# Kernel optimization log

Measured on AMD Instinct MI355X. Metric: run time of the kernel, lower is better.

Reference implementation:

```python
import jax, jax.numpy as jnp
import numpy as np

H = 10  # hidden_dim

def _lstm_layer(x_tbd, w_ih, w_hh, b_ih, b_hh):
    # x_tbd: [T, B, D]; w_ih: [4H, D]; w_hh: [4H, H]; biases [4H]
    B = x_tbd.shape[1]
    h0 = jnp.zeros((B, H), x_tbd.dtype)
    c0 = jnp.zeros((B, H), x_tbd.dtype)
    # precompute input projections for all timesteps: [T, B, 4H]
    xg = jnp.einsum('tbd,gd->tbg', x_tbd, w_ih) + b_ih + b_hh

    def step(carry, xg_t):
        h, c = carry
        gates = xg_t + h @ w_hh.T  # [B, 4H]
        i, f, g, o = jnp.split(gates, 4, axis=-1)  # torch gate order i,f,g,o
        i = jax.nn.sigmoid(i); f = jax.nn.sigmoid(f)
        g = jnp.tanh(g); o = jax.nn.sigmoid(o)
        c = f * c + i * g
        h = o * jnp.tanh(c)
        return (h, c), h

    (hT, cT), hs = jax.lax.scan(step, (h0, c0), xg)
    return hs, hT  # hs: [T, B, H]

def setup_inputs() -> dict:
    key = jax.random.key(0)
    ks = jax.random.split(key, 11)
    B, T, D = 32768, 28, 28
    s0 = 1.0 / np.sqrt(H)
    u = lambda k, shape: jax.random.uniform(k, shape, jnp.float32, -s0, s0)
    return {
        'x': jax.random.normal(ks[0], (B, T, D), jnp.float32),
        'w_ih0': u(ks[1], (4 * H, D)),
        'w_hh0': u(ks[2], (4 * H, H)),
        'b_ih0': u(ks[3], (4 * H,)),
        'b_hh0': u(ks[4], (4 * H,)),
        'w_ih1': u(ks[5], (4 * H, H)),
        'w_hh1': u(ks[6], (4 * H, H)),
        'b_ih1': u(ks[7], (4 * H,)),
        'b_hh1': u(ks[8], (4 * H,)),
        'w_cls': u(ks[9], (10, H)),
        'b_cls': u(ks[10], (10,)),
    }

def reference(x, w_ih0, w_hh0, b_ih0, b_hh0, w_ih1, w_hh1, b_ih1, b_hh1, w_cls, b_cls):
    x_tbd = jnp.swapaxes(x, 0, 1)  # [T, B, D]
    hs0, _ = _lstm_layer(x_tbd, w_ih0, w_hh0, b_ih0, b_hh0)
    _, hT1 = _lstm_layer(hs0, w_ih1, w_hh1, b_ih1, b_hh1)  # hT1 = h_n[-1]
    return hT1 @ w_cls.T + b_cls  # [B, 10]
```

## Files before the change

### kernel.cpp

```cpp
#include <hip/hip_runtime.h>


#define HDIM 10
#define DDIM 28
#define TSTEPS 28

typedef __attribute__((ext_vector_type(8))) short short8;
typedef __attribute__((ext_vector_type(4))) float f32x4;

__device__ __forceinline__ unsigned short bf16_rne(float f) {
    unsigned u = __builtin_bit_cast(unsigned, f);
    u += 0x7FFFu + ((u >> 16) & 1u);
    return (unsigned short)(u >> 16);
}
__device__ __forceinline__ float bf16_f(unsigned short h) {
    unsigned u = ((unsigned)h) << 16;
    return __builtin_bit_cast(float, u);
}
__device__ __forceinline__ unsigned pk_hl(float v) {
    unsigned a, p;
    const float z = 0.0f;
    asm("v_cvt_pk_bf16_f32 %0, %1, %2" : "=v"(a) : "v"(v), "v"(z));
    const float hif = __builtin_bit_cast(float, a << 16);
    const float d = v - hif;
    asm("v_cvt_pk_bf16_f32 %0, %1, %2" : "=v"(p) : "v"(v), "v"(d));
    return p;
}
__device__ __forceinline__ float sig_f(float v) {
    return __builtin_amdgcn_rcpf(1.0f + __expf(-v));
}
__device__ __forceinline__ float act_eval(float v, float a) {
    return a * __builtin_amdgcn_rcpf(1.0f + __expf(-a * v)) + (1.0f - a);
}
__device__ __forceinline__ float tanh_f(float v) {
    return 2.0f * __builtin_amdgcn_rcpf(1.0f + __expf(-2.0f * v)) - 1.0f;
}

#define FENCE() __asm volatile("" ::: "memory")
#define WR32(arrp, sidx, val) (*(unsigned*)&(arrp)[(sidx)] = (val))

__global__ __launch_bounds__(64) void lstm2_mfma_kernel(
    const float* __restrict__ x,
    const float* __restrict__ w_ih0, const float* __restrict__ w_hh0,
    const float* __restrict__ b_ih0, const float* __restrict__ b_hh0,
    const float* __restrict__ w_ih1, const float* __restrict__ w_hh1,
    const float* __restrict__ b_ih1, const float* __restrict__ b_hh1,
    const float* __restrict__ w_cls, const float* __restrict__ b_cls,
    float* __restrict__ out)
{
    __shared__ unsigned short uA0[16 * 136];
    __shared__ unsigned short uA1[16 * 72];
    __shared__ float gb[2][48 * 20];
    __shared__ float hfin[16 * 12];

    const int l  = threadIdx.x;
    const int lm = l & 15;
    const int q  = l >> 4;
    const int sbase = blockIdx.x * 16;

    for (int i = l; i < 16 * 22; i += 64) uA0[(i / 22) * 136 + 114 + (i % 22)] = 0;
    for (int i = l; i < 16 * 12; i += 64) uA1[(i / 12) * 72 + 60 + (i % 12)] = 0;

    short8 B0[3][4], B1[3][2];
    #pragma unroll
    for (int T = 0; T < 3; ++T) {
        const int n = lm + 16 * T;
        #pragma unroll
        for (int c = 0; c < 4; ++c) {
            #pragma unroll
            for (int j = 0; j < 8; ++j) {
                const int kk = 32 * c + 8 * q + j;
                unsigned short bits = 0;
                if (n < 40 && kk < 114) {
                    if (kk < 76) {
                        const int j2 = kk >> 1;
                        const float w = (j2 < 28) ? w_ih0[n * 28 + j2]
                                                  : w_hh0[n * 10 + (j2 - 28)];
                        bits = bf16_rne(w);
                    } else {
                        const int d = kk - 76;
                        const float w = (d < 28) ? w_ih0[n * 28 + d]
                                                 : w_hh0[n * 10 + (d - 28)];
                        const unsigned short hi = bf16_rne(w);
                        bits = bf16_rne(w - bf16_f(hi));
                    }
                }
                B0[T][c][j] = (short)bits;
            }
        }
        #pragma unroll
        for (int c = 0; c < 2; ++c) {
            #pragma unroll
            for (int j = 0; j < 8; ++j) {
                const int kk = 32 * c + 8 * q + j;
                unsigned short bits = 0;
                if (n < 40 && kk < 60) {
                    if (kk < 40) {
                        const int j2 = kk >> 1;
                        const float w = (j2 < 10) ? w_ih1[n * 10 + j2]
                                                  : w_hh1[n * 10 + (j2 - 10)];
                        bits = bf16_rne(w);
                    } else {
                        const int d = kk - 40;
                        const float w = (d < 10) ? w_ih1[n * 10 + d]
                                                 : w_hh1[n * 10 + (d - 10)];
                        const unsigned short hi = bf16_rne(w);
                        bits = bf16_rne(w - bf16_f(hi));
                    }
                }
                B1[T][c][j] = (short)bits;
            }
        }
    }

    float bias0[3], bias1[3];
    #pragma unroll
    for (int T = 0; T < 3; ++T) {
        const int n = lm + 16 * T;
        bias0[T] = (n < 40) ? (b_ih0[n] + b_hh0[n]) : 0.0f;
        bias1[T] = (n < 40) ? (b_ih1[n] + b_hh1[n]) : 0.0f;
    }
    const float a1v = (lm >= 4 && lm < 14) ? 2.0f : 1.0f;

    int xoff[7], lofsA[7], lofsB[7]; float xn[7];
    #pragma unroll
    for (int i = 0; i < 7; ++i) {
        const int f = l + 64 * i;
        const int sm = f / 28, d = f - 28 * sm;
        lofsA[i] = sm * 136 + 2 * d;
        lofsB[i] = sm * 136 + 76 + d;
        xoff[i] = (sbase + sm) * (TSTEPS * DDIM) + d;
        xn[i] = x[xoff[i]];
    }
    #pragma unroll
    for (int i = 0; i < 7; ++i) {
        const unsigned p = pk_hl(xn[i]);
        WR32(uA0, lofsA[i], p);
        uA0[lofsB[i]] = (unsigned short)p;
    }
    if (lm < 10) {
        #pragma unroll
        for (int r = 0; r < 4; ++r) {
            const int m = 4 * q + r;
            unsigned short* r0 = &uA0[m * 136];
            WR32(r0, 56 + 2 * lm, 0u); r0[104 + lm] = 0;
            unsigned short* r1 = &uA1[m * 72];
            WR32(r1, 2 * lm, 0u);      r1[40 + lm] = 0;
            WR32(r1, 20 + 2 * lm, 0u); r1[50 + lm] = 0;
        }
    }
    FENCE();

    float c0s[4] = {0, 0, 0, 0}, c1s[4] = {0, 0, 0, 0};
    float h1v[4] = {0, 0, 0, 0};
    float h0v[4];
    short8 A0f[4], A1f[2];
    float* const gb0 = gb[0];
    float* const gb1 = gb[1];

    #pragma unroll
    for (int c = 0; c < 4; ++c)
        A0f[c] = *(const short8*)&uA0[lm * 136 + 32 * c + 8 * q];
    FENCE();
    #pragma unroll
    for (int i = 0; i < 7; ++i) { xoff[i] += DDIM; xn[i] = x[xoff[i]]; }
    {
        f32x4 C[3];
        #pragma unroll
        for (int T = 0; T < 3; ++T) {
            f32x4 acc = {bias0[T], bias0[T], bias0[T], bias0[T]};
            #pragma unroll
            for (int c = 0; c < 4; ++c)
                acc = __builtin_amdgcn_mfma_f32_16x16x32_bf16(A0f[c], B0[T][c], acc, 0, 0, 0);
            C[T] = acc;
        }
        f32x4 g0, g1t, g2;
        #pragma unroll
        for (int r = 0; r < 4; ++r) {
            g0[r]  = sig_f(C[0][r]);
            g1t[r] = act_eval(C[1][r], a1v);
            g2[r]  = sig_f(C[2][r]);
        }
        *(f32x4*)&gb0[(lm     ) * 20 + 4 * q] = g0;
        *(f32x4*)&gb0[(lm + 16) * 20 + 4 * q] = g1t;
        *(f32x4*)&gb0[(lm + 32) * 20 + 4 * q] = g2;
    }
    FENCE();
    {
        const f32x4 iv = *(const f32x4*)&gb0[(lm     ) * 20 + 4 * q];
        const f32x4 fv = *(const f32x4*)&gb0[(lm + 10) * 20 + 4 * q];
        const f32x4 gg = *(const f32x4*)&gb0[(lm + 20) * 20 + 4 * q];
        const f32x4 ov = *(const f32x4*)&gb0[(lm + 30) * 20 + 4 * q];
        #pragma unroll
        for (int r = 0; r < 4; ++r) {
            const float c = fv[r] * c0s[r] + iv[r] * gg[r];
            c0s[r] = c;
            h0v[r] = ov[r] * tanh_f(c);
        }
        if (lm < 10) {
            #pragma unroll
            for (int r = 0; r < 4; ++r) {
                const int m = 4 * q + r;
                const unsigned p0 = pk_hl(h0v[r]);
                unsigned short* r0 = &uA0[m * 136];
                WR32(r0, 56 + 2 * lm, p0); r0[104 + lm] = (unsigned short)p0;
                unsigned short* r1 = &uA1[m * 72];
                WR32(r1, 2 * lm, p0);      r1[40 + lm] = (unsigned short)p0;
            }
        }
        #pragma unroll
        for (int i = 0; i < 7; ++i) {
            const unsigned p = pk_hl(xn[i]);
            WR32(uA0, lofsA[i], p);
            uA0[lofsB[i]] = (unsigned short)p;
        }
    }
    FENCE();

    #pragma unroll 1
    for (int t = 0; t < TSTEPS - 1; ++t) {
        #pragma unroll
        for (int c = 0; c < 2; ++c)
            A1f[c] = *(const short8*)&uA1[lm * 72 + 32 * c + 8 * q];
        #pragma unroll
        for (int c = 0; c < 4; ++c)
            A0f[c] = *(const short8*)&uA0[lm * 136 + 32 * c + 8 * q];
        FENCE();

        if (t < TSTEPS - 2) {
            #pragma unroll
            for (int i = 0; i < 7; ++i) { xoff[i] += DDIM; xn[i] = x[xoff[i]]; }
        }

        f32x4 C[3], D[3];
        #pragma unroll
        for (int T = 0; T < 3; ++T) {
            f32x4 accD = {bias1[T], bias1[T], bias1[T], bias1[T]};
            #pragma unroll
            for (int c = 0; c < 2; ++c)
                accD = __builtin_amdgcn_mfma_f32_16x16x32_bf16(A1f[c], B1[T][c], accD, 0, 0, 0);
            D[T] = accD;
            f32x4 accC = {bias0[T], bias0[T], bias0[T], bias0[T]};
            #pragma unroll
            for (int c = 0; c < 4; ++c)
                accC = __builtin_amdgcn_mfma_f32_16x16x32_bf16(A0f[c], B0[T][c], accC, 0, 0, 0);
            C[T] = accC;
        }

        {
            f32x4 d0, d1, d2, e0, e1, e2;
            #pragma unroll
            for (int r = 0; r < 4; ++r) {
                d0[r] = sig_f(D[0][r]);
                d1[r] = act_eval(D[1][r], a1v);
                d2[r] = sig_f(D[2][r]);
                e0[r] = sig_f(C[0][r]);
                e1[r] = act_eval(C[1][r], a1v);
                e2[r] = sig_f(C[2][r]);
            }
            *(f32x4*)&gb1[(lm     ) * 20 + 4 * q] = d0;
            *(f32x4*)&gb1[(lm + 16) * 20 + 4 * q] = d1;
            *(f32x4*)&gb1[(lm + 32) * 20 + 4 * q] = d2;
            *(f32x4*)&gb0[(lm     ) * 20 + 4 * q] = e0;
            *(f32x4*)&gb0[(lm + 16) * 20 + 4 * q] = e1;
            *(f32x4*)&gb0[(lm + 32) * 20 + 4 * q] = e2;
        }
        FENCE();

        {
            const f32x4 iv1 = *(const f32x4*)&gb1[(lm     ) * 20 + 4 * q];
            const f32x4 fv1 = *(const f32x4*)&gb1[(lm + 10) * 20 + 4 * q];
            const f32x4 gg1 = *(const f32x4*)&gb1[(lm + 20) * 20 + 4 * q];
            const f32x4 ov1 = *(const f32x4*)&gb1[(lm + 30) * 20 + 4 * q];
            const f32x4 iv0 = *(const f32x4*)&gb0[(lm     ) * 20 + 4 * q];
            const f32x4 fv0 = *(const f32x4*)&gb0[(lm + 10) * 20 + 4 * q];
            const f32x4 gg0 = *(const f32x4*)&gb0[(lm + 20) * 20 + 4 * q];
            const f32x4 ov0 = *(const f32x4*)&gb0[(lm + 30) * 20 + 4 * q];
            #pragma unroll
            for (int r = 0; r < 4; ++r) {
                const float c1 = fv1[r] * c1s[r] + iv1[r] * gg1[r];
                c1s[r] = c1;
                h1v[r] = ov1[r] * tanh_f(c1);
                const float c0 = fv0[r] * c0s[r] + iv0[r] * gg0[r];
                c0s[r] = c0;
                h0v[r] = ov0[r] * tanh_f(c0);
            }
            if (lm < 10) {
                #pragma unroll
                for (int r = 0; r < 4; ++r) {
                    const int m = 4 * q + r;
                    const unsigned p1 = pk_hl(h1v[r]);
                    unsigned short* r1 = &uA1[m * 72];
                    WR32(r1, 20 + 2 * lm, p1); r1[50 + lm] = (unsigned short)p1;
                    const unsigned p0 = pk_hl(h0v[r]);
                    WR32(r1, 2 * lm, p0);      r1[40 + lm] = (unsigned short)p0;
                    unsigned short* r0 = &uA0[m * 136];
                    WR32(r0, 56 + 2 * lm, p0); r0[104 + lm] = (unsigned short)p0;
                }
            }
            if (t < TSTEPS - 2) {
                #pragma unroll
                for (int i = 0; i < 7; ++i) {
                    const unsigned p = pk_hl(xn[i]);
                    WR32(uA0, lofsA[i], p);
                    uA0[lofsB[i]] = (unsigned short)p;
                }
            }
        }
        FENCE();
    }

    {
        #pragma unroll
        for (int c = 0; c < 2; ++c)
            A1f[c] = *(const short8*)&uA1[lm * 72 + 32 * c + 8 * q];
        FENCE();
        f32x4 D[3];
        #pragma unroll
        for (int T = 0; T < 3; ++T) {
            f32x4 acc = {bias1[T], bias1[T], bias1[T], bias1[T]};
            #pragma unroll
            for (int c = 0; c < 2; ++c)
                acc = __builtin_amdgcn_mfma_f32_16x16x32_bf16(A1f[c], B1[T][c], acc, 0, 0, 0);
            D[T] = acc;
        }
        f32x4 d0, d1, d2;
        #pragma unroll
        for (int r = 0; r < 4; ++r) {
            d0[r] = sig_f(D[0][r]);
            d1[r] = act_eval(D[1][r], a1v);
            d2[r] = sig_f(D[2][r]);
        }
        *(f32x4*)&gb1[(lm     ) * 20 + 4 * q] = d0;
        *(f32x4*)&gb1[(lm + 16) * 20 + 4 * q] = d1;
        *(f32x4*)&gb1[(lm + 32) * 20 + 4 * q] = d2;
        FENCE();
        const f32x4 iv = *(const f32x4*)&gb1[(lm     ) * 20 + 4 * q];
        const f32x4 fv = *(const f32x4*)&gb1[(lm + 10) * 20 + 4 * q];
        const f32x4 gg = *(const f32x4*)&gb1[(lm + 20) * 20 + 4 * q];
        const f32x4 ov = *(const f32x4*)&gb1[(lm + 30) * 20 + 4 * q];
        #pragma unroll
        for (int r = 0; r < 4; ++r) {
            const float c = fv[r] * c1s[r] + iv[r] * gg[r];
            h1v[r] = ov[r] * tanh_f(c);
        }
    }

    if (lm < 10) {
        #pragma unroll
        for (int r = 0; r < 4; ++r) hfin[(4 * q + r) * 12 + lm] = h1v[r];
    }
    FENCE();
    if (lm < 10) {
        float wc[10];
        #pragma unroll
        for (int j = 0; j < 10; ++j) wc[j] = w_cls[lm * 10 + j];
        const float bo = b_cls[lm];
        #pragma unroll
        for (int r = 0; r < 4; ++r) {
            const int m = 4 * q + r;
            float acc = bo;
            #pragma unroll
            for (int j = 0; j < 10; ++j) acc += hfin[m * 12 + j] * wc[j];
            out[(size_t)(sbase + m) * 10 + lm] = acc;
        }
    }
}

extern "C" void kernel_launch(void* const* d_in, const int* in_sizes, int n_in,
                              void* d_out, int out_size, void* d_ws, size_t ws_size,
                              hipStream_t stream) {
    const float* x     = (const float*)d_in[0];
    const float* w_ih0 = (const float*)d_in[1];
    const float* w_hh0 = (const float*)d_in[2];
    const float* b_ih0 = (const float*)d_in[3];
    const float* b_hh0 = (const float*)d_in[4];
    const float* w_ih1 = (const float*)d_in[5];
    const float* w_hh1 = (const float*)d_in[6];
    const float* b_ih1 = (const float*)d_in[7];
    const float* b_hh1 = (const float*)d_in[8];
    const float* w_cls = (const float*)d_in[9];
    const float* b_cls = (const float*)d_in[10];
    float* out = (float*)d_out;

    const int B = in_sizes[0] / (TSTEPS * DDIM);
    const int grid = B / 16;

    hipLaunchKernelGGL(lstm2_mfma_kernel, dim3(grid), dim3(64), 0, stream,
                       x, w_ih0, w_hh0, b_ih0, b_hh0,
                       w_ih1, w_hh1, b_ih1, b_hh1,
                       w_cls, b_cls, out);
}
```

Before: 261.8 us.

## Remap gate columns so each lane holds all four gates, drop LDS gate exchange

Reorganizes the MFMA B-operand so that N-tile T holds gate T for hidden units 0..9 in lanes lm<10, giving each lane i,f,g,o in registers. This removes the per-step shared-memory round trip (store gates, fence, reload) and the blended act_eval trick. In exchange it issues four MFMA tiles per layer instead of three, a third more matrix work, and computes activations on six idle lanes per 16.

```diff
diff --git a/kernel.cpp b/kernel.cpp
--- a/kernel.cpp
+++ b/kernel.cpp
@@ -28,9 +28,6 @@
 }
 __device__ __forceinline__ float sig_f(float v) {
     return __builtin_amdgcn_rcpf(1.0f + __expf(-v));
-}
-__device__ __forceinline__ float act_eval(float v, float a) {
-    return a * __builtin_amdgcn_rcpf(1.0f + __expf(-a * v)) + (1.0f - a);
 }
 __device__ __forceinline__ float tanh_f(float v) {
     return 2.0f * __builtin_amdgcn_rcpf(1.0f + __expf(-2.0f * v)) - 1.0f;
@@ -50,7 +47,6 @@
 {
     __shared__ unsigned short uA0[16 * 136];
     __shared__ unsigned short uA1[16 * 72];
-    __shared__ float gb[2][48 * 20];
     __shared__ float hfin[16 * 12];
 
     const int l  = threadIdx.x;
@@ -61,26 +57,27 @@
     for (int i = l; i < 16 * 22; i += 64) uA0[(i / 22) * 136 + 114 + (i % 22)] = 0;
     for (int i = l; i < 16 * 12; i += 64) uA1[(i / 12) * 72 + 60 + (i % 12)] = 0;
 
-    short8 B0[3][4], B1[3][2];
-    #pragma unroll
-    for (int T = 0; T < 3; ++T) {
-        const int n = lm + 16 * T;
+    short8 B0[4][4], B1[4][2];
+    const bool gvalid = (lm < 10);
+    #pragma unroll
+    for (int T = 0; T < 4; ++T) {
+        const int g = 10 * T + lm;
         #pragma unroll
         for (int c = 0; c < 4; ++c) {
             #pragma unroll
             for (int j = 0; j < 8; ++j) {
                 const int kk = 32 * c + 8 * q + j;
                 unsigned short bits = 0;
-                if (n < 40 && kk < 114) {
+                if (gvalid && kk < 114) {
                     if (kk < 76) {
                         const int j2 = kk >> 1;
-                        const float w = (j2 < 28) ? w_ih0[n * 28 + j2]
-                                                  : w_hh0[n * 10 + (j2 - 28)];
+                        const float w = (j2 < 28) ? w_ih0[g * 28 + j2]
+                                                  : w_hh0[g * 10 + (j2 - 28)];
                         bits = bf16_rne(w);
                     } else {
                         const int d = kk - 76;
-                        const float w = (d < 28) ? w_ih0[n * 28 + d]
-                                                 : w_hh0[n * 10 + (d - 28)];
+                        const float w = (d < 28) ? w_ih0[g * 28 + d]
+                                                 : w_hh0[g * 10 + (d - 28)];
                         const unsigned short hi = bf16_rne(w);
                         bits = bf16_rne(w - bf16_f(hi));
                     }
@@ -94,16 +91,16 @@
             for (int j = 0; j < 8; ++j) {
                 const int kk = 32 * c + 8 * q + j;
                 unsigned short bits = 0;
-                if (n < 40 && kk < 60) {
+                if (gvalid && kk < 60) {
                     if (kk < 40) {
                         const int j2 = kk >> 1;
-                        const float w = (j2 < 10) ? w_ih1[n * 10 + j2]
-                                                  : w_hh1[n * 10 + (j2 - 10)];
+                        const float w = (j2 < 10) ? w_ih1[g * 10 + j2]
+                                                  : w_hh1[g * 10 + (j2 - 10)];
                         bits = bf16_rne(w);
                     } else {
                         const int d = kk - 40;
-                        const float w = (d < 10) ? w_ih1[n * 10 + d]
-                                                 : w_hh1[n * 10 + (d - 10)];
+                        const float w = (d < 10) ? w_ih1[g * 10 + d]
+                                                 : w_hh1[g * 10 + (d - 10)];
                         const unsigned short hi = bf16_rne(w);
                         bits = bf16_rne(w - bf16_f(hi));
                     }
@@ -113,14 +110,13 @@
         }
     }
 
-    float bias0[3], bias1[3];
-    #pragma unroll
-    for (int T = 0; T < 3; ++T) {
-        const int n = lm + 16 * T;
-        bias0[T] = (n < 40) ? (b_ih0[n] + b_hh0[n]) : 0.0f;
-        bias1[T] = (n < 40) ? (b_ih1[n] + b_hh1[n]) : 0.0f;
-    }
-    const float a1v = (lm >= 4 && lm < 14) ? 2.0f : 1.0f;
+    float bias0[4], bias1[4];
+    #pragma unroll
+    for (int T = 0; T < 4; ++T) {
+        const int g = 10 * T + lm;
+        bias0[T] = gvalid ? (b_ih0[g] + b_hh0[g]) : 0.0f;
+        bias1[T] = gvalid ? (b_ih1[g] + b_hh1[g]) : 0.0f;
+    }
 
     int xoff[7], lofsA[7], lofsB[7]; float xn[7];
     #pragma unroll
@@ -155,8 +151,6 @@
     float h1v[4] = {0, 0, 0, 0};
     float h0v[4];
     short8 A0f[4], A1f[2];
-    float* const gb0 = gb[0];
-    float* const gb1 = gb[1];
 
     #pragma unroll
     for (int c = 0; c < 4; ++c)
@@ -165,37 +159,24 @@
     #pragma unroll
     for (int i = 0; i < 7; ++i) { xoff[i] += DDIM; xn[i] = x[xoff[i]]; }
     {
-        f32x4 C[3];
-        #pragma unroll
-        for (int T = 0; T < 3; ++T) {
+        f32x4 C[4];
+        #pragma unroll
+        for (int T = 0; T < 4; ++T) {
             f32x4 acc = {bias0[T], bias0[T], bias0[T], bias0[T]};
             #pragma unroll
             for (int c = 0; c < 4; ++c)
                 acc = __builtin_amdgcn_mfma_f32_16x16x32_bf16(A0f[c], B0[T][c], acc, 0, 0, 0);
             C[T] = acc;
         }
-        f32x4 g0, g1t, g2;
-        #pragma unroll
-        for (int r = 0; r < 4; ++r) {
-            g0[r]  = sig_f(C[0][r]);
-            g1t[r] = act_eval(C[1][r], a1v);
-            g2[r]  = sig_f(C[2][r]);
-        }
-        *(f32x4*)&gb0[(lm     ) * 20 + 4 * q] = g0;
-        *(f32x4*)&gb0[(lm + 16) * 20 + 4 * q] = g1t;
-        *(f32x4*)&gb0[(lm + 32) * 20 + 4 * q] = g2;
-    }
-    FENCE();
-    {
-        const f32x4 iv = *(const f32x4*)&gb0[(lm     ) * 20 + 4 * q];
-        const f32x4 fv = *(const f32x4*)&gb0[(lm + 10) * 20 + 4 * q];
-        const f32x4 gg = *(const f32x4*)&gb0[(lm + 20) * 20 + 4 * q];
-        const f32x4 ov = *(const f32x4*)&gb0[(lm + 30) * 20 + 4 * q];
-        #pragma unroll
-        for (int r = 0; r < 4; ++r) {
-            const float c = fv[r] * c0s[r] + iv[r] * gg[r];
-            c0s[r] = c;
-            h0v[r] = ov[r] * tanh_f(c);
+        #pragma unroll
+        for (int r = 0; r < 4; ++r) {
+            const float i0 = sig_f(C[0][r]);
+            const float f0 = sig_f(C[1][r]);
+            const float g0 = tanh_f(C[2][r]);
+            const float o0 = sig_f(C[3][r]);
+            const float c0 = f0 * c0s[r] + i0 * g0;
+            c0s[r] = c0;
+            h0v[r] = o0 * tanh_f(c0);
         }
         if (lm < 10) {
             #pragma unroll
@@ -232,9 +213,9 @@
             for (int i = 0; i < 7; ++i) { xoff[i] += DDIM; xn[i] = x[xoff[i]]; }
         }
 
-        f32x4 C[3], D[3];
-        #pragma unroll
-        for (int T = 0; T < 3; ++T) {
+        f32x4 C[4], D[4];
+        #pragma unroll
+        for (int T = 0; T < 4; ++T) {
             f32x4 accD = {bias1[T], bias1[T], bias1[T], bias1[T]};
             #pragma unroll
             for (int c = 0; c < 2; ++c)
@@ -247,64 +228,43 @@
             C[T] = accC;
         }
 
-        {
-            f32x4 d0, d1, d2, e0, e1, e2;
+        #pragma unroll
+        for (int r = 0; r < 4; ++r) {
+            const float i1 = sig_f(D[0][r]);
+            const float f1 = sig_f(D[1][r]);
+            const float g1 = tanh_f(D[2][r]);
+            const float o1 = sig_f(D[3][r]);
+            const float c1 = f1 * c1s[r] + i1 * g1;
+            c1s[r] = c1;
+            h1v[r] = o1 * tanh_f(c1);
+            const float i0 = sig_f(C[0][r]);
+            const float f0 = sig_f(C[1][r]);
+            const float g0 = tanh_f(C[2][r]);
+            const float o0 = sig_f(C[3][r]);
+            const float c0 = f0 * c0s[r] + i0 * g0;
+            c0s[r] = c0;
+            h0v[r] = o0 * tanh_f(c0);
+        }
+
+        if (lm < 10) {
             #pragma unroll
             for (int r = 0; r < 4; ++r) {
-                d0[r] = sig_f(D[0][r]);
-                d1[r] = act_eval(D[1][r], a1v);
-                d2[r] = sig_f(D[2][r]);
-                e0[r] = sig_f(C[0][r]);
-                e1[r] = act_eval(C[1][r], a1v);
-                e2[r] = sig_f(C[2][r]);
-            }
-            *(f32x4*)&gb1[(lm     ) * 20 + 4 * q] = d0;
-            *(f32x4*)&gb1[(lm + 16) * 20 + 4 * q] = d1;
-            *(f32x4*)&gb1[(lm + 32) * 20 + 4 * q] = d2;
-            *(f32x4*)&gb0[(lm     ) * 20 + 4 * q] = e0;
-            *(f32x4*)&gb0[(lm + 16) * 20 + 4 * q] = e1;
-            *(f32x4*)&gb0[(lm + 32) * 20 + 4 * q] = e2;
-        }
-        FENCE();
-
-        {
-            const f32x4 iv1 = *(const f32x4*)&gb1[(lm     ) * 20 + 4 * q];
-            const f32x4 fv1 = *(const f32x4*)&gb1[(lm + 10) * 20 + 4 * q];
-            const f32x4 gg1 = *(const f32x4*)&gb1[(lm + 20) * 20 + 4 * q];
-            const f32x4 ov1 = *(const f32x4*)&gb1[(lm + 30) * 20 + 4 * q];
-            const f32x4 iv0 = *(const f32x4*)&gb0[(lm     ) * 20 + 4 * q];
-            const f32x4 fv0 = *(const f32x4*)&gb0[(lm + 10) * 20 + 4 * q];
-            const f32x4 gg0 = *(const f32x4*)&gb0[(lm + 20) * 20 + 4 * q];
-            const f32x4 ov0 = *(const f32x4*)&gb0[(lm + 30) * 20 + 4 * q];
-            #pragma unroll
-            for (int r = 0; r < 4; ++r) {
-                const float c1 = fv1[r] * c1s[r] + iv1[r] * gg1[r];
-                c1s[r] = c1;
-                h1v[r] = ov1[r] * tanh_f(c1);
-                const float c0 = fv0[r] * c0s[r] + iv0[r] * gg0[r];
-                c0s[r] = c0;
-                h0v[r] = ov0[r] * tanh_f(c0);
-            }
-            if (lm < 10) {
-                #pragma unroll
-                for (int r = 0; r < 4; ++r) {
-                    const int m = 4 * q + r;
-                    const unsigned p1 = pk_hl(h1v[r]);
-                    unsigned short* r1 = &uA1[m * 72];
-                    WR32(r1, 20 + 2 * lm, p1); r1[50 + lm] = (unsigned short)p1;
-                    const unsigned p0 = pk_hl(h0v[r]);
-                    WR32(r1, 2 * lm, p0);      r1[40 + lm] = (unsigned short)p0;
-                    unsigned short* r0 = &uA0[m * 136];
-                    WR32(r0, 56 + 2 * lm, p0); r0[104 + lm] = (unsigned short)p0;
-                }
-            }
-            if (t < TSTEPS - 2) {
-                #pragma unroll
-                for (int i = 0; i < 7; ++i) {
-                    const unsigned p = pk_hl(xn[i]);
-                    WR32(uA0, lofsA[i], p);
-                    uA0[lofsB[i]] = (unsigned short)p;
-                }
+                const int m = 4 * q + r;
+                const unsigned p1 = pk_hl(h1v[r]);
+                unsigned short* r1 = &uA1[m * 72];
+                WR32(r1, 20 + 2 * lm, p1); r1[50 + lm] = (unsigned short)p1;
+                const unsigned p0 = pk_hl(h0v[r]);
+                WR32(r1, 2 * lm, p0);      r1[40 + lm] = (unsigned short)p0;
+                unsigned short* r0 = &uA0[m * 136];
+                WR32(r0, 56 + 2 * lm, p0); r0[104 + lm] = (unsigned short)p0;
+            }
+        }
+        if (t < TSTEPS - 2) {
+            #pragma unroll
+            for (int i = 0; i < 7; ++i) {
+                const unsigned p = pk_hl(xn[i]);
+                WR32(uA0, lofsA[i], p);
+                uA0[lofsB[i]] = (unsigned short)p;
             }
         }
         FENCE();
@@ -315,34 +275,23 @@
         for (int c = 0; c < 2; ++c)
             A1f[c] = *(const short8*)&uA1[lm * 72 + 32 * c + 8 * q];
         FENCE();
-        f32x4 D[3];
-        #pragma unroll
-        for (int T = 0; T < 3; ++T) {
+        f32x4 D[4];
+        #pragma unroll
+        for (int T = 0; T < 4; ++T) {
             f32x4 acc = {bias1[T], bias1[T], bias1[T], bias1[T]};
             #pragma unroll
             for (int c = 0; c < 2; ++c)
                 acc = __builtin_amdgcn_mfma_f32_16x16x32_bf16(A1f[c], B1[T][c], acc, 0, 0, 0);
             D[T] = acc;
         }
-        f32x4 d0, d1, d2;
-        #pragma unroll
-        for (int r = 0; r < 4; ++r) {
-            d0[r] = sig_f(D[0][r]);
-            d1[r] = act_eval(D[1][r], a1v);
-            d2[r] = sig_f(D[2][r]);
-        }
-        *(f32x4*)&gb1[(lm     ) * 20 + 4 * q] = d0;
-        *(f32x4*)&gb1[(lm + 16) * 20 + 4 * q] = d1;
-        *(f32x4*)&gb1[(lm + 32) * 20 + 4 * q] = d2;
-        FENCE();
-        const f32x4 iv = *(const f32x4*)&gb1[(lm     ) * 20 + 4 * q];
-        const f32x4 fv = *(const f32x4*)&gb1[(lm + 10) * 20 + 4 * q];
-        const f32x4 gg = *(const f32x4*)&gb1[(lm + 20) * 20 + 4 * q];
-        const f32x4 ov = *(const f32x4*)&gb1[(lm + 30) * 20 + 4 * q];
-        #pragma unroll
-        for (int r = 0; r < 4; ++r) {
-            const float c = fv[r] * c1s[r] + iv[r] * gg[r];
-            h1v[r] = ov[r] * tanh_f(c);
+        #pragma unroll
+        for (int r = 0; r < 4; ++r) {
+            const float i1 = sig_f(D[0][r]);
+            const float f1 = sig_f(D[1][r]);
+            const float g1 = tanh_f(D[2][r]);
+            const float o1 = sig_f(D[3][r]);
+            const float c1 = f1 * c1s[r] + i1 * g1;
+            h1v[r] = o1 * tanh_f(c1);
         }
     }
 
```

Result: slower. 268.4 us (+2.5%).
